# Kernel tuning notes

Measured on AMD Instinct MI355X. Metric: run time of the kernel, lower is better.

## Reference

```python
import jax, jax.numpy as jnp
import numpy as np

B, Q, LE, D, P, A = 8, 32, 128, 512, 32, 128


def setup_inputs() -> dict:
    key = jax.random.key(0)
    ks = jax.random.split(key, 8)
    exp_tokens = jax.random.normal(ks[0], (B, Q, LE, D), dtype=jnp.float32)
    exp_mask = jax.random.randint(ks[1], (B, Q, LE), 0, 2, dtype=jnp.int32)
    s_j = jax.random.normal(ks[2], (B, P, D), dtype=jnp.float32)
    req_mask = jax.random.randint(ks[3], (B, P), 0, 2, dtype=jnp.int32)
    sc = 1.0 / np.sqrt(D)
    Ws_w = jax.random.normal(ks[4], (A, D), dtype=jnp.float32) * sc
    Ws_b = jax.random.normal(ks[5], (A,), dtype=jnp.float32) * 0.01
    U_w = jax.random.normal(ks[6], (A, D), dtype=jnp.float32) * sc
    v_w = jax.random.normal(ks[7], (1, A), dtype=jnp.float32) * (1.0 / np.sqrt(A))
    return {"exp_tokens": exp_tokens, "exp_mask": exp_mask, "s_j": s_j,
            "req_mask": req_mask, "Ws_w": Ws_w, "Ws_b": Ws_b, "U_w": U_w, "v_w": v_w}


def reference(exp_tokens, exp_mask, s_j, req_mask, Ws_w, Ws_b, U_w, v_w):
    # ws: (B,P,A); uh: (B,Q,Le,A)
    ws = jnp.einsum('bpd,ad->bpa', s_j, Ws_w) + Ws_b
    uh = jnp.einsum('bqtd,ad->bqta', exp_tokens, U_w)
    # broadcast add -> (B,Q,P,Le,A), tanh, project with v -> (B,Q,P,Le)
    scored = jnp.tanh(uh[:, :, None, :, :] + ws[:, None, :, None, :])
    e = jnp.einsum('bqpta,a->bqpt', scored, v_w[0])
    tok_mask = exp_mask[:, :, None, :]  # (B,Q,1,Le) broadcast over P
    e = jnp.where(tok_mask == 0, jnp.float32(-1e9), e)
    # joint softmax over Q*Le per (b,p)
    e_t = jnp.transpose(e, (0, 2, 1, 3)).reshape(e.shape[0], e.shape[2], -1)
    a = jax.nn.softmax(e_t, axis=-1).reshape(e.shape[0], e.shape[2], e.shape[1], e.shape[3])
    a = jnp.transpose(a, (0, 2, 1, 3))  # (B,Q,P,Le)
    s_rlk = jnp.einsum('bqpt,bqtd->bqpd', a, exp_tokens)
    rmask = req_mask[:, None, :, None].astype(s_rlk.dtype)
    return s_rlk * rmask
```

## Files before the change

kernel.cpp:

```cpp
#include <hip/hip_runtime.h>
#include <hip/hip_bf16.h>

#define B_  8
#define Q_  32
#define LE_ 128
#define D_  512
#define P_  32
#define A_  128

typedef __attribute__((ext_vector_type(8))) short short8_t;
typedef __attribute__((ext_vector_type(4))) float floatx4_t;

typedef const __attribute__((address_space(1))) unsigned int glb_uint;
typedef __attribute__((address_space(3))) unsigned int lds_uint;
#define GLD16(g, s) __builtin_amdgcn_global_load_lds((glb_uint*)(g), (lds_uint*)(s), 16, 0, 0)

__device__ __forceinline__ short f2bf(float x) {
    unsigned u = __float_as_uint(x);
    unsigned r = (u + 0x7fffu + ((u >> 16) & 1u)) >> 16;
    return (short)r;
}
__device__ __forceinline__ float bf2f(short s) {
    return __uint_as_float(((unsigned)(unsigned short)s) << 16);
}

__global__ __launch_bounds__(256) void convert_kernel(
    const float* __restrict__ X, const float* __restrict__ W,
    short* __restrict__ Xb, short* __restrict__ Wb) {
    int b = blockIdx.x;
    const float* src;
    short* dst;
    size_t base;
    if (b < 8192) {
        base = ((size_t)b * 256 + threadIdx.x) * 8;
        src = X + base; dst = Xb + base;
    } else {
        base = ((size_t)(b - 8192) * 256 + threadIdx.x) * 8;
        src = W + base; dst = Wb + base;
    }
    float4 v0 = ((const float4*)src)[0];
    float4 v1 = ((const float4*)src)[1];
    short8_t s;
    s[0] = f2bf(v0.x); s[1] = f2bf(v0.y); s[2] = f2bf(v0.z); s[3] = f2bf(v0.w);
    s[4] = f2bf(v1.x); s[5] = f2bf(v1.y); s[6] = f2bf(v1.z); s[7] = f2bf(v1.w);
    *(short8_t*)dst = s;
}

__global__ __launch_bounds__(128) void ws_kernel(
    const float* __restrict__ s_j, const float* __restrict__ Ws_w,
    const float* __restrict__ Ws_b, float* __restrict__ ws) {
    __shared__ float s_row[D_];
    int bp = blockIdx.x;
    const float* src = s_j + (size_t)bp * D_;
    for (int i = threadIdx.x; i < D_; i += 128) s_row[i] = src[i];
    __syncthreads();
    int a = threadIdx.x;
    const float4* w4 = (const float4*)(Ws_w + (size_t)a * D_);
    const float4* s4 = (const float4*)s_row;
    float acc = 0.0f;
#pragma unroll 8
    for (int i = 0; i < D_ / 4; ++i) {
        float4 w = w4[i];
        float4 s = s4[i];
        acc += w.x * s.x + w.y * s.y + w.z * s.z + w.w * s.w;
    }
    ws[bp * A_ + a] = __expf(2.0f * (acc + Ws_b[a]));
}

#define EUP_ 136
#define EWP_ 132
#define WPP_ 136

__global__ __launch_bounds__(512, 1) void fused_kernel(
    const short* __restrict__ Xb, const short* __restrict__ Wb,
    const float* __restrict__ EW, const float* __restrict__ v_w,
    const int* __restrict__ exp_mask, float* __restrict__ gsums,
    float* __restrict__ out) {
    __shared__ short uA[128 * EUP_];
    __shared__ float ew_s[32 * EWP_];
    __shared__ short w_s[32 * WPP_];
    __shared__ float n2v[128];
    __shared__ int   mask_s[128];

    int bq = blockIdx.x;
    int b  = bq >> 5;
    int tid = threadIdx.x;
    int wave = tid >> 6, lane = tid & 63;
    int qd = lane >> 4, lr = lane & 15;

    short* As = uA;
    short* Bs = uA + 8192;

    int m0 = (wave >> 1) * 32, n0 = (wave & 1) * 64;
    int cA = lane & 7;
    int row0 = wave * 16 + (lane >> 3);

    floatx4_t acc[2][4];
#pragma unroll
    for (int i = 0; i < 2; ++i)
#pragma unroll
        for (int j = 0; j < 4; ++j) acc[i][j] = (floatx4_t){0.f, 0.f, 0.f, 0.f};

    for (int kt = 0; kt < 8; ++kt) {
        int k0 = kt * 64;
        __syncthreads();
#pragma unroll
        for (int u = 0; u < 2; ++u) {
            int m = row0 + u * 8;
            GLD16(Xb + (size_t)(bq * 128 + m) * D_ + k0 + ((cA ^ (m & 7)) * 8),
                  As + (wave * 2 + u) * 512);
        }
#pragma unroll
        for (int u = 0; u < 2; ++u) {
            int n = row0 + u * 8;
            GLD16(Wb + (size_t)n * D_ + k0 + ((cA ^ (n & 7)) * 8),
                  Bs + (wave * 2 + u) * 512);
        }
        __syncthreads();
#pragma unroll
        for (int ks = 0; ks < 2; ++ks) {
            int cr = (ks * 4 + qd) ^ (lr & 7);
            short8_t af[2], bfr[4];
#pragma unroll
            for (int i = 0; i < 2; ++i)
                af[i] = *(const short8_t*)(As + (m0 + i * 16 + lr) * 64 + cr * 8);
#pragma unroll
            for (int j = 0; j < 4; ++j)
                bfr[j] = *(const short8_t*)(Bs + (n0 + j * 16 + lr) * 64 + cr * 8);
#pragma unroll
            for (int i = 0; i < 2; ++i)
#pragma unroll
                for (int j = 0; j < 4; ++j)
                    acc[i][j] = __builtin_amdgcn_mfma_f32_16x16x32_bf16(af[i], bfr[j], acc[i][j], 0, 0, 0);
        }
    }
    __syncthreads();

#pragma unroll
    for (int i = 0; i < 2; ++i)
#pragma unroll
        for (int j = 0; j < 4; ++j)
#pragma unroll
            for (int r = 0; r < 4; ++r) {
                int t = m0 + i * 16 + qd * 4 + r;
                int a = n0 + j * 16 + lr;
                uA[t * EUP_ + a] = f2bf(__expf(2.0f * acc[i][j][r]));
            }
#pragma unroll
    for (int u = 0; u < 2; ++u) {
        int c = tid * 2 + u;
        int p = c >> 5, seg = c & 31;
        *(float4*)&ew_s[p * EWP_ + seg * 4] =
            *(const float4*)&EW[(size_t)(b * P_ + p) * A_ + seg * 4];
    }
    if (tid < 32) {
        float4 v = *(const float4*)(v_w + tid * 4);
        v.x *= -2.0f; v.y *= -2.0f; v.z *= -2.0f; v.w *= -2.0f;
        *(float4*)&n2v[tid * 4] = v;
    }
    if (tid < 128) mask_s[tid] = exp_mask[bq * LE_ + tid];
    __syncthreads();

    {
        int t = tid & 127, pg = tid >> 7;
        float acc8[8];
#pragma unroll
        for (int j = 0; j < 8; ++j) acc8[j] = 0.0f;
        for (int a8 = 0; a8 < 16; ++a8) {
            short8_t e8 = *(const short8_t*)&uA[t * EUP_ + a8 * 8];
            float eu[8];
#pragma unroll
            for (int k = 0; k < 8; ++k) eu[k] = bf2f(e8[k]);
            float4 nv0 = *(const float4*)&n2v[a8 * 8];
            float4 nv1 = *(const float4*)&n2v[a8 * 8 + 4];
            float nv[8] = {nv0.x, nv0.y, nv0.z, nv0.w, nv1.x, nv1.y, nv1.z, nv1.w};
#pragma unroll
            for (int j = 0; j < 8; ++j) {
                int p = pg * 8 + j;
                float4 w0 = *(const float4*)&ew_s[p * EWP_ + a8 * 8];
                float4 w1 = *(const float4*)&ew_s[p * EWP_ + a8 * 8 + 4];
                float ww[8] = {w0.x, w0.y, w0.z, w0.w, w1.x, w1.y, w1.z, w1.w};
#pragma unroll
                for (int k = 0; k < 8; ++k)
                    acc8[j] = fmaf(nv[k], __builtin_amdgcn_rcpf(fmaf(eu[k], ww[k], 1.0f)), acc8[j]);
            }
        }
        int mk = mask_s[t];
#pragma unroll
        for (int j = 0; j < 8; ++j) {
            float ee = mk ? __expf(acc8[j]) : 0.0f;
            w_s[(pg * 8 + j) * WPP_ + t] = f2bf(ee);
        }
    }
    __syncthreads();

    if (tid < 256) {
        int p = tid >> 3, seg = tid & 7;
        const short* src = w_s + p * WPP_ + seg * 16;
        float s = 0.0f;
#pragma unroll
        for (int k = 0; k < 16; ++k) s += bf2f(src[k]);
        s += __shfl_xor(s, 1);
        s += __shfl_xor(s, 2);
        s += __shfl_xor(s, 4);
        if (seg == 0) atomicAdd(&gsums[b * P_ + p], s);
    }

    short8_t afv[2][4];
#pragma unroll
    for (int i = 0; i < 2; ++i)
#pragma unroll
        for (int ks = 0; ks < 4; ++ks)
            afv[i][ks] = *(const short8_t*)&w_s[(i * 16 + lr) * WPP_ + ks * 32 + qd * 8];

    int tt = tid >> 2, dseg = (tid & 3) * 32;
    for (int chunk = 0; chunk < 4; ++chunk) {
        int d0 = chunk * 128;
        __syncthreads();
        const short8_t* g = (const short8_t*)(Xb + (size_t)(bq * 128 + tt) * D_ + d0 + dseg);
        short8_t xs0 = g[0], xs1 = g[1], xs2 = g[2], xs3 = g[3];
#pragma unroll
        for (int e = 0; e < 8; ++e) {
            uA[(dseg + 0 + e) * EUP_ + tt]  = xs0[e];
            uA[(dseg + 8 + e) * EUP_ + tt]  = xs1[e];
            uA[(dseg + 16 + e) * EUP_ + tt] = xs2[e];
            uA[(dseg + 24 + e) * EUP_ + tt] = xs3[e];
        }
        __syncthreads();
        floatx4_t accp[2];
        accp[0] = (floatx4_t){0.f, 0.f, 0.f, 0.f};
        accp[1] = (floatx4_t){0.f, 0.f, 0.f, 0.f};
#pragma unroll
        for (int ks = 0; ks < 4; ++ks) {
            short8_t bfr = *(const short8_t*)&uA[(wave * 16 + lr) * EUP_ + ks * 32 + qd * 8];
            accp[0] = __builtin_amdgcn_mfma_f32_16x16x32_bf16(afv[0][ks], bfr, accp[0], 0, 0, 0);
            accp[1] = __builtin_amdgcn_mfma_f32_16x16x32_bf16(afv[1][ks], bfr, accp[1], 0, 0, 0);
        }
#pragma unroll
        for (int i = 0; i < 2; ++i)
#pragma unroll
            for (int r = 0; r < 4; ++r) {
                int p = i * 16 + qd * 4 + r;
                out[((size_t)bq * P_ + p) * D_ + d0 + wave * 16 + lr] = accp[i][r];
            }
    }
}

__global__ __launch_bounds__(256) void norm_kernel(
    float* __restrict__ out, const float* __restrict__ gsums,
    const int* __restrict__ req_mask) {
    int bqp = blockIdx.x;
    int p = bqp & 31;
    int b = bqp >> 10;
    int bp = b * P_ + p;
    float s = gsums[bp];
    float rm = req_mask[bp] ? __fdividef(1.0f, s) : 0.0f;
    float2* o = (float2*)(out + (size_t)bqp * D_);
    float2 v = o[threadIdx.x];
    v.x *= rm; v.y *= rm;
    o[threadIdx.x] = v;
}

extern "C" void kernel_launch(void* const* d_in, const int* in_sizes, int n_in,
                              void* d_out, int out_size, void* d_ws, size_t ws_size,
                              hipStream_t stream) {
    const float* exp_tokens = (const float*)d_in[0];
    const int*   exp_mask   = (const int*)d_in[1];
    const float* s_j        = (const float*)d_in[2];
    const int*   req_mask   = (const int*)d_in[3];
    const float* Ws_w       = (const float*)d_in[4];
    const float* Ws_b       = (const float*)d_in[5];
    const float* U_w        = (const float*)d_in[6];
    const float* v_w        = (const float*)d_in[7];
    float* out = (float*)d_out;

    float* EW    = (float*)d_ws;
    float* gsums = EW + B_ * P_ * A_;
    short* Xb    = (short*)(gsums + 256);
    short* Wb    = Xb + (size_t)B_ * Q_ * LE_ * D_;

    hipMemsetAsync(gsums, 0, B_ * P_ * sizeof(float), stream);
    convert_kernel<<<dim3(8192 + 32), dim3(256), 0, stream>>>(exp_tokens, U_w, Xb, Wb);
    ws_kernel<<<dim3(B_ * P_), dim3(128), 0, stream>>>(s_j, Ws_w, Ws_b, EW);
    fused_kernel<<<dim3(B_ * Q_), dim3(512), 0, stream>>>(Xb, Wb, EW, v_w, exp_mask, gsums, out);
    norm_kernel<<<dim3(B_ * Q_ * P_), dim3(256), 0, stream>>>(out, gsums, req_mask);
}
```

Baseline: 169.6 us.

## Emit transposed bf16 tokens in convert kernel and stage PV operand via async LDS loads

The convert kernel now also writes a transposed bf16 copy of the tokens (per bq, D-major) through an LDS tile. The fused kernel's PV GEMM uses it to load B operands straight into LDS with global_load_lds and an XOR swizzle, replacing the scalar LDS transposes. The prefetch of the next chunk is issued after each compute step. The first GEMM's K tile also grows from 64 to 128, and shared memory is unified into an arena. This adds an extra 32MB write of transposed data in exchange for removing in-kernel transposes.

Result: slower. 181.8 us (+7.2%).

```diff
diff --git a/kernel.cpp b/kernel.cpp
--- a/kernel.cpp
+++ b/kernel.cpp
@@ -24,26 +24,46 @@
     return __uint_as_float(((unsigned)(unsigned short)s) << 16);
 }
 
+#define TP_ 136
 __global__ __launch_bounds__(256) void convert_kernel(
     const float* __restrict__ X, const float* __restrict__ W,
-    short* __restrict__ Xb, short* __restrict__ Wb) {
-    int b = blockIdx.x;
-    const float* src;
-    short* dst;
-    size_t base;
-    if (b < 8192) {
-        base = ((size_t)b * 256 + threadIdx.x) * 8;
-        src = X + base; dst = Xb + base;
-    } else {
-        base = ((size_t)(b - 8192) * 256 + threadIdx.x) * 8;
-        src = W + base; dst = Wb + base;
-    }
-    float4 v0 = ((const float4*)src)[0];
-    float4 v1 = ((const float4*)src)[1];
-    short8_t s;
-    s[0] = f2bf(v0.x); s[1] = f2bf(v0.y); s[2] = f2bf(v0.z); s[3] = f2bf(v0.w);
-    s[4] = f2bf(v1.x); s[5] = f2bf(v1.y); s[6] = f2bf(v1.z); s[7] = f2bf(v1.w);
-    *(short8_t*)dst = s;
+    short* __restrict__ Xb, short* __restrict__ XbT, short* __restrict__ Wb) {
+    int blk = blockIdx.x;
+    int tid = threadIdx.x;
+    if (blk >= 1024) {
+        size_t base = (size_t)(blk - 1024) * 2048 + tid * 8;
+        float4 v0 = ((const float4*)(W + base))[0];
+        float4 v1 = ((const float4*)(W + base))[1];
+        short8_t s;
+        s[0] = f2bf(v0.x); s[1] = f2bf(v0.y); s[2] = f2bf(v0.z); s[3] = f2bf(v0.w);
+        s[4] = f2bf(v1.x); s[5] = f2bf(v1.y); s[6] = f2bf(v1.z); s[7] = f2bf(v1.w);
+        *(short8_t*)(Wb + base) = s;
+        return;
+    }
+    __shared__ short tile[128 * TP_];
+    int bq = blk >> 2, d0 = (blk & 3) * 128;
+    int tt = tid >> 5, dd = (tid & 31) * 4;
+#pragma unroll 4
+    for (int pass = 0; pass < 16; ++pass) {
+        int t = tt + pass * 8;
+        float4 v = *(const float4*)(X + (size_t)(bq * LE_ + t) * D_ + d0 + dd);
+        unsigned s0 = (unsigned short)f2bf(v.x), s1 = (unsigned short)f2bf(v.y);
+        unsigned s2 = (unsigned short)f2bf(v.z), s3 = (unsigned short)f2bf(v.w);
+        uint2 pk;
+        pk.x = s0 | (s1 << 16);
+        pk.y = s2 | (s3 << 16);
+        *(uint2*)(Xb + (size_t)(bq * LE_ + t) * D_ + d0 + dd) = pk;
+        tile[(dd + 0) * TP_ + t] = (short)s0;
+        tile[(dd + 1) * TP_ + t] = (short)s1;
+        tile[(dd + 2) * TP_ + t] = (short)s2;
+        tile[(dd + 3) * TP_ + t] = (short)s3;
+    }
+    __syncthreads();
+    int dr = tid >> 1, th = (tid & 1) * 64;
+    short* dst = XbT + ((size_t)(bq * D_) + d0 + dr) * LE_ + th;
+#pragma unroll
+    for (int i = 0; i < 8; ++i)
+        *(short8_t*)(dst + i * 8) = *(const short8_t*)(tile + dr * TP_ + th + i * 8);
 }
 
 __global__ __launch_bounds__(128) void ws_kernel(
@@ -73,14 +93,19 @@
 
 __global__ __launch_bounds__(512, 1) void fused_kernel(
     const short* __restrict__ Xb, const short* __restrict__ Wb,
+    const short* __restrict__ XbT,
     const float* __restrict__ EW, const float* __restrict__ v_w,
     const int* __restrict__ exp_mask, float* __restrict__ gsums,
     float* __restrict__ out) {
-    __shared__ short uA[128 * EUP_];
-    __shared__ float ew_s[32 * EWP_];
-    __shared__ short w_s[32 * WPP_];
-    __shared__ float n2v[128];
-    __shared__ int   mask_s[128];
+    __shared__ __align__(16) char arena[65536];
+    short* stgA  = (short*)arena;
+    short* stgB  = (short*)(arena + 32768);
+    short* EU    = (short*)arena;
+    float* ew_s  = (float*)(arena + 34816);
+    short* w_s   = (short*)(arena + 51712);
+    float* n2v   = (float*)(arena + 60416);
+    int*   mask_s= (int*)(arena + 60928);
+    short* pvB   = (short*)arena;
 
     int bq = blockIdx.x;
     int b  = bq >> 5;
@@ -88,12 +113,9 @@
     int wave = tid >> 6, lane = tid & 63;
     int qd = lane >> 4, lr = lane & 15;
 
-    short* As = uA;
-    short* Bs = uA + 8192;
-
     int m0 = (wave >> 1) * 32, n0 = (wave & 1) * 64;
-    int cA = lane & 7;
-    int row0 = wave * 16 + (lane >> 3);
+    int rsub = lane >> 4;
+    int slot = lane & 15;
 
     floatx4_t acc[2][4];
 #pragma unroll
@@ -101,32 +123,29 @@
 #pragma unroll
         for (int j = 0; j < 4; ++j) acc[i][j] = (floatx4_t){0.f, 0.f, 0.f, 0.f};
 
-    for (int kt = 0; kt < 8; ++kt) {
-        int k0 = kt * 64;
+    for (int kt = 0; kt < 4; ++kt) {
+        int k0 = kt * 128;
         __syncthreads();
 #pragma unroll
-        for (int u = 0; u < 2; ++u) {
-            int m = row0 + u * 8;
-            GLD16(Xb + (size_t)(bq * 128 + m) * D_ + k0 + ((cA ^ (m & 7)) * 8),
-                  As + (wave * 2 + u) * 512);
-        }
-#pragma unroll
-        for (int u = 0; u < 2; ++u) {
-            int n = row0 + u * 8;
-            GLD16(Wb + (size_t)n * D_ + k0 + ((cA ^ (n & 7)) * 8),
-                  Bs + (wave * 2 + u) * 512);
+        for (int u = 0; u < 4; ++u) {
+            int row = wave * 16 + u * 4 + rsub;
+            int sc = (slot ^ (row & 15)) * 8;
+            GLD16(Xb + (size_t)(bq * 128 + row) * D_ + k0 + sc,
+                  stgA + (wave * 16 + u * 4) * 128);
+            GLD16(Wb + (size_t)row * D_ + k0 + sc,
+                  stgB + (wave * 16 + u * 4) * 128);
         }
         __syncthreads();
 #pragma unroll
-        for (int ks = 0; ks < 2; ++ks) {
-            int cr = (ks * 4 + qd) ^ (lr & 7);
+        for (int ks = 0; ks < 4; ++ks) {
+            int co = ((ks * 4 + qd) ^ lr) * 8;
             short8_t af[2], bfr[4];
 #pragma unroll
             for (int i = 0; i < 2; ++i)
-                af[i] = *(const short8_t*)(As + (m0 + i * 16 + lr) * 64 + cr * 8);
+                af[i] = *(const short8_t*)(stgA + (m0 + i * 16 + lr) * 128 + co);
 #pragma unroll
             for (int j = 0; j < 4; ++j)
-                bfr[j] = *(const short8_t*)(Bs + (n0 + j * 16 + lr) * 64 + cr * 8);
+                bfr[j] = *(const short8_t*)(stgB + (n0 + j * 16 + lr) * 128 + co);
 #pragma unroll
             for (int i = 0; i < 2; ++i)
 #pragma unroll
@@ -144,7 +163,7 @@
             for (int r = 0; r < 4; ++r) {
                 int t = m0 + i * 16 + qd * 4 + r;
                 int a = n0 + j * 16 + lr;
-                uA[t * EUP_ + a] = f2bf(__expf(2.0f * acc[i][j][r]));
+                EU[t * EUP_ + a] = f2bf(__expf(2.0f * acc[i][j][r]));
             }
 #pragma unroll
     for (int u = 0; u < 2; ++u) {
@@ -167,7 +186,7 @@
 #pragma unroll
         for (int j = 0; j < 8; ++j) acc8[j] = 0.0f;
         for (int a8 = 0; a8 < 16; ++a8) {
-            short8_t e8 = *(const short8_t*)&uA[t * EUP_ + a8 * 8];
+            short8_t e8 = *(const short8_t*)&EU[t * EUP_ + a8 * 8];
             float eu[8];
 #pragma unroll
             for (int k = 0; k < 8; ++k) eu[k] = bf2f(e8[k]);
@@ -194,6 +213,17 @@
     }
     __syncthreads();
 
+    auto stage4 = [&](int chunk) {
+#pragma unroll
+        for (int u = 0; u < 4; ++u) {
+            int row = wave * 16 + u * 4 + rsub;
+            int sc = (slot ^ (row & 15)) * 8;
+            GLD16(XbT + ((size_t)(bq * D_) + chunk * 128 + row) * LE_ + sc,
+                  pvB + (wave * 16 + u * 4) * 128);
+        }
+    };
+    stage4(0);
+
     if (tid < 256) {
         int p = tid >> 3, seg = tid & 7;
         const short* src = w_s + p * WPP_ + seg * 16;
@@ -213,26 +243,15 @@
         for (int ks = 0; ks < 4; ++ks)
             afv[i][ks] = *(const short8_t*)&w_s[(i * 16 + lr) * WPP_ + ks * 32 + qd * 8];
 
-    int tt = tid >> 2, dseg = (tid & 3) * 32;
     for (int chunk = 0; chunk < 4; ++chunk) {
-        int d0 = chunk * 128;
-        __syncthreads();
-        const short8_t* g = (const short8_t*)(Xb + (size_t)(bq * 128 + tt) * D_ + d0 + dseg);
-        short8_t xs0 = g[0], xs1 = g[1], xs2 = g[2], xs3 = g[3];
-#pragma unroll
-        for (int e = 0; e < 8; ++e) {
-            uA[(dseg + 0 + e) * EUP_ + tt]  = xs0[e];
-            uA[(dseg + 8 + e) * EUP_ + tt]  = xs1[e];
-            uA[(dseg + 16 + e) * EUP_ + tt] = xs2[e];
-            uA[(dseg + 24 + e) * EUP_ + tt] = xs3[e];
-        }
         __syncthreads();
         floatx4_t accp[2];
         accp[0] = (floatx4_t){0.f, 0.f, 0.f, 0.f};
         accp[1] = (floatx4_t){0.f, 0.f, 0.f, 0.f};
 #pragma unroll
         for (int ks = 0; ks < 4; ++ks) {
-            short8_t bfr = *(const short8_t*)&uA[(wave * 16 + lr) * EUP_ + ks * 32 + qd * 8];
+            int co = ((ks * 4 + qd) ^ lr) * 8;
+            short8_t bfr = *(const short8_t*)&pvB[(wave * 16 + lr) * 128 + co];
             accp[0] = __builtin_amdgcn_mfma_f32_16x16x32_bf16(afv[0][ks], bfr, accp[0], 0, 0, 0);
             accp[1] = __builtin_amdgcn_mfma_f32_16x16x32_bf16(afv[1][ks], bfr, accp[1], 0, 0, 0);
         }
@@ -241,8 +260,12 @@
 #pragma unroll
             for (int r = 0; r < 4; ++r) {
                 int p = i * 16 + qd * 4 + r;
-                out[((size_t)bq * P_ + p) * D_ + d0 + wave * 16 + lr] = accp[i][r];
+                out[((size_t)bq * P_ + p) * D_ + chunk * 128 + wave * 16 + lr] = accp[i][r];
             }
+        if (chunk < 3) {
+            __syncthreads();
+            stage4(chunk + 1);
+        }
     }
 }
 
@@ -277,11 +300,12 @@
     float* EW    = (float*)d_ws;
     float* gsums = EW + B_ * P_ * A_;
     short* Xb    = (short*)(gsums + 256);
-    short* Wb    = Xb + (size_t)B_ * Q_ * LE_ * D_;
+    short* XbT   = Xb + (size_t)B_ * Q_ * LE_ * D_;
+    short* Wb    = XbT + (size_t)B_ * Q_ * LE_ * D_;
 
     hipMemsetAsync(gsums, 0, B_ * P_ * sizeof(float), stream);
-    convert_kernel<<<dim3(8192 + 32), dim3(256), 0, stream>>>(exp_tokens, U_w, Xb, Wb);
+    convert_kernel<<<dim3(1024 + 32), dim3(256), 0, stream>>>(exp_tokens, U_w, Xb, XbT, Wb);
     ws_kernel<<<dim3(B_ * P_), dim3(128), 0, stream>>>(s_j, Ws_w, Ws_b, EW);
-    fused_kernel<<<dim3(B_ * Q_), dim3(512), 0, stream>>>(Xb, Wb, EW, v_w, exp_mask, gsums, out);
+    fused_kernel<<<dim3(B_ * Q_), dim3(512), 0, stream>>>(Xb, Wb, XbT, EW, v_w, exp_mask, gsums, out);
     norm_kernel<<<dim3(B_ * Q_ * P_), dim3(256), 0, stream>>>(out, gsums, req_mask);
 }
```
